# Kernel tuning notes

Hardware: AMD Instinct MI355X
Metric: run time of the kernel (lower is better)

Reference implementation:

```python
import jax, jax.numpy as jnp
import numpy as np
from jax import lax

B, N, G, K = 32, 8192, 512, 32
CH = [64, 128, 256]
EPS = 1e-5


def setup_inputs() -> dict:
    key = jax.random.key(0)
    ks = jax.random.split(key, 8)
    inp = {"points": jax.random.normal(ks[0], (B, N, 3), dtype=jnp.float32)}
    last = 3
    for li, c in enumerate(CH):
        inp[f"w{li}"] = jax.random.normal(ks[li + 1], (c, last), jnp.float32) * (1.0 / np.sqrt(last))
        inp[f"b{li}"] = jnp.zeros((c,), jnp.float32)
        inp[f"gamma{li}"] = jnp.ones((c,), jnp.float32)
        inp[f"beta{li}"] = jnp.zeros((c,), jnp.float32)
        inp[f"mean{li}"] = jnp.zeros((c,), jnp.float32)
        inp[f"var{li}"] = jnp.ones((c,), jnp.float32)
        last = c
    return inp


def _fps(xyz, npoint):
    # farthest point sampling: xyz [B,N,3] -> indices [B, npoint]
    b, n, _ = xyz.shape
    first = jnp.zeros((b,), jnp.int32)

    def step(carry, _):
        mindist, last_idx = carry
        last = jnp.take_along_axis(xyz, last_idx[:, None, None], axis=1)  # [B,1,3]
        d = jnp.sum((xyz - last) ** 2, axis=-1)  # [B,N]
        mindist = jnp.minimum(mindist, d)
        nxt = jnp.argmax(mindist, axis=-1).astype(jnp.int32)
        return (mindist, nxt), nxt

    init = (jnp.full((b, n), 1e10, jnp.float32), first)
    _, rest = lax.scan(step, init, None, length=npoint - 1)  # [npoint-1, B]
    return jnp.concatenate([first[None, :], rest], axis=0).T  # [B, npoint]


def _sample_and_group(points):
    idx_c = _fps(points, G)                                           # [B,G]
    centers = jnp.take_along_axis(points, idx_c[..., None], axis=1)   # [B,G,3]
    # kNN: squared distance [B,G,N]
    d = jnp.sum((centers[:, :, None, :] - points[:, None, :, :]) ** 2, axis=-1)
    _, idx = lax.top_k(-d, K)                                         # [B,G,K]
    grouped = jax.vmap(lambda p, i: p[i])(points, idx)                # [B,G,K,3]
    neighborhoods = grouped - centers[:, :, None, :]                  # recenter
    return neighborhoods, centers


def _mlp_maxpool(neigh, layers):
    h = neigh  # [B,G,K,C]
    for (w, b, g, be, m, v) in layers:
        h = jnp.einsum('bgkc,oc->bgko', h, w) + b       # 1x1 conv == linear
        h = (h - m) * (g / jnp.sqrt(v + EPS)) + be      # BatchNorm (inference)
        h = jax.nn.relu(h)
    return jnp.max(h, axis=(1, 2))                      # max over K then G == max over both


def reference(points, w0, b0, gamma0, beta0, mean0, var0,
              w1, b1, gamma1, beta1, mean1, var1,
              w2, b2, gamma2, beta2, mean2, var2):
    neigh, _ = _sample_and_group(points)
    layers = [(w0, b0, gamma0, beta0, mean0, var0),
              (w1, b1, gamma1, beta1, mean1, var1),
              (w2, b2, gamma2, beta2, mean2, var2)]
    return _mlp_maxpool(neigh, layers)  # [B, 256]
```

## Files before the change

### kernel.cpp

```cpp
#include <hip/hip_runtime.h>

#define B_ 32
#define N_ 8192
#define G_ 512
#define K_ 32
#define EPSF 1e-5f

typedef __attribute__((ext_vector_type(8))) short bf16x8;
typedef __attribute__((ext_vector_type(4))) float f32x4;
typedef __attribute__((ext_vector_type(2))) float f32x2;
typedef __attribute__((ext_vector_type(2))) unsigned long long u64x2;

static __device__ __forceinline__ short f2bf(float f) {
    unsigned u = __float_as_uint(f);
    u += 0x7fffu + ((u >> 16) & 1u);
    return (short)(u >> 16);
}

static __device__ __forceinline__ unsigned long long u64max(unsigned long long a,
                                                            unsigned long long b) {
    return a > b ? a : b;
}
static __device__ __forceinline__ unsigned long long u64min(unsigned long long a,
                                                            unsigned long long b) {
    return a < b ? a : b;
}

template <int CTL>
static __device__ __forceinline__ unsigned long long dpp_shr_u64(unsigned long long k) {
    const int lo = __builtin_amdgcn_mov_dpp((int)(unsigned)k, CTL, 0xf, 0xf, true);
    const int hi = __builtin_amdgcn_mov_dpp((int)(unsigned)(k >> 32), CTL, 0xf, 0xf, true);
    return ((unsigned long long)(unsigned)hi << 32) | (unsigned)lo;
}

template <int CTL>
static __device__ __forceinline__ unsigned long long dpp_upd_u64(unsigned long long k) {
    const int lo = __builtin_amdgcn_update_dpp((int)(unsigned)k, (int)(unsigned)k,
                                               CTL, 0xf, 0xf, false);
    const int hi = __builtin_amdgcn_update_dpp((int)(unsigned)(k >> 32),
                                               (int)(unsigned)(k >> 32),
                                               CTL, 0xf, 0xf, false);
    return ((unsigned long long)(unsigned)hi << 32) | (unsigned)lo;
}

__global__ __launch_bounds__(256) void prep_kernel(
    const float* __restrict__ w0, const float* __restrict__ b0,
    const float* __restrict__ g0, const float* __restrict__ be0,
    const float* __restrict__ m0, const float* __restrict__ v0,
    const float* __restrict__ w1, const float* __restrict__ b1,
    const float* __restrict__ g1, const float* __restrict__ be1,
    const float* __restrict__ m1, const float* __restrict__ v1,
    const float* __restrict__ w2, const float* __restrict__ b2,
    const float* __restrict__ g2, const float* __restrict__ be2,
    const float* __restrict__ m2, const float* __restrict__ v2,
    float* __restrict__ W0b, float* __restrict__ b1b, float* __restrict__ b2b,
    short* __restrict__ W1b, short* __restrict__ W2b) {
    const int t = threadIdx.x;
    if (t < 64) {
        const float sc = g0[t] / sqrtf(v0[t] + EPSF);
        W0b[t * 4 + 0] = w0[t * 3 + 0] * sc;
        W0b[t * 4 + 1] = w0[t * 3 + 1] * sc;
        W0b[t * 4 + 2] = w0[t * 3 + 2] * sc;
        W0b[t * 4 + 3] = (b0[t] - m0[t]) * sc + be0[t];
    }
    if (t < 128) b1b[t] = (b1[t] - m1[t]) * (g1[t] / sqrtf(v1[t] + EPSF)) + be1[t];
    if (t < 256) b2b[t] = (b2[t] - m2[t]) * (g2[t] / sqrtf(v2[t] + EPSF)) + be2[t];
    for (int i = t; i < 128 * 64; i += 256) {
        const int o = i >> 6;
        const float sc = g1[o] / sqrtf(v1[o] + EPSF);
        W1b[i] = f2bf(w1[i] * sc);
    }
    for (int i = t; i < 256 * 128; i += 256) {
        const int o = i >> 7;
        const float sc = g2[o] / sqrtf(v2[o] + EPSF);
        W2b[i] = f2bf(w2[i] * sc);
    }
}

__global__ __launch_bounds__(256) void fps_kernel(const float* __restrict__ pts,
                                                  float* __restrict__ centers) {
    __shared__ float4 sxyz[N_];
    __shared__ __align__(16) unsigned long long rowkeys[2][16];

    const int b = blockIdx.x;
    const int t = threadIdx.x;
    const int l = t & 63;
    const int w = t >> 6;
    const float* p = pts + (size_t)b * (N_ * 3);

    f32x2 px[16], py[16], pz[16], md[16];
#pragma unroll
    for (int i = 0; i < 16; ++i) {
        const int i0 = t + (2 * i) * 256;
        const int i1 = i0 + 256;
        px[i] = f32x2{p[3 * i0 + 0], p[3 * i1 + 0]};
        py[i] = f32x2{p[3 * i0 + 1], p[3 * i1 + 1]};
        pz[i] = f32x2{p[3 * i0 + 2], p[3 * i1 + 2]};
        sxyz[i0] = make_float4(px[i][0], py[i][0], pz[i][0], 0.0f);
        sxyz[i1] = make_float4(px[i][1], py[i][1], pz[i][1], 0.0f);
        md[i] = f32x2{1e10f, 1e10f};
    }
    __syncthreads();

    if (t == 0) {
        float* c = centers + (size_t)b * (G_ * 3);
        c[0] = px[0][0]; c[1] = py[0][0]; c[2] = pz[0][0];
    }
    const float4 c0 = sxyz[0];
    float lx = c0.x, ly = c0.y, lz = c0.z;
    const int pay0 = 8191 - t;

    for (int g = 1; g < G_; ++g) {
        const f32x2 nlx = {-lx, -lx};
        const f32x2 nly = {-ly, -ly};
        const f32x2 nlz = {-lz, -lz};
        float m_best = -1.0f;
        int j_best = 0;
        {
#pragma clang fp contract(off)
#pragma unroll
            for (int i = 0; i < 16; ++i) {
                const f32x2 dx = px[i] + nlx;
                const f32x2 dy = py[i] + nly;
                const f32x2 dz = pz[i] + nlz;
                const f32x2 d = (dx * dx + dy * dy) + dz * dz;
                const f32x2 m = __builtin_elementwise_min(md[i], d);
                md[i] = m;
                const bool c0_ = m[0] > m_best;
                m_best = c0_ ? m[0] : m_best;
                j_best = c0_ ? 2 * i : j_best;
                const bool c1_ = m[1] > m_best;
                m_best = c1_ ? m[1] : m_best;
                j_best = c1_ ? 2 * i + 1 : j_best;
            }
        }
        unsigned long long key =
            ((unsigned long long)__float_as_uint(m_best) << 13) |
            (unsigned long long)(unsigned)(pay0 - (j_best << 8));

        key = u64max(key, dpp_shr_u64<0x111>(key));
        key = u64max(key, dpp_shr_u64<0x112>(key));
        key = u64max(key, dpp_shr_u64<0x114>(key));
        key = u64max(key, dpp_shr_u64<0x118>(key));
        if ((l & 15) == 15) rowkeys[g & 1][w * 4 + (l >> 4)] = key;
        __syncthreads();

        const u64x2* rk = (const u64x2*)&rowkeys[g & 1][0];
        const u64x2 k2 = rk[l & 7];
        unsigned long long kk = u64max(k2[0], k2[1]);
        kk = u64max(kk, dpp_shr_u64<0x111>(kk));
        kk = u64max(kk, dpp_shr_u64<0x112>(kk));
        kk = u64max(kk, dpp_shr_u64<0x114>(kk));
        const unsigned blo =
            (unsigned)__builtin_amdgcn_readlane((int)(unsigned)kk, 7);
        const int last = 8191 - (int)(blo & 0x1FFFu);

        const float4 cc = sxyz[last];
        lx = cc.x; ly = cc.y; lz = cc.z;
        if (t == 0) {
            float* c = centers + ((size_t)b * G_ + g) * 3;
            c[0] = lx; c[1] = ly; c[2] = lz;
        }
    }
}

__global__ __launch_bounds__(256) void knn_kernel(const float* __restrict__ pts,
                                                  const float* __restrict__ centers,
                                                  float* __restrict__ neigh) {
    __shared__ unsigned long long wkeys[4][32];
    __shared__ int midx[32];

    const int cid = blockIdx.x;
    const int b = cid >> 9;
    const int t = threadIdx.x;
    const int w = t >> 6;
    const int l = t & 63;
    const float* p = pts + (size_t)b * (N_ * 3);
    const float* c = centers + (size_t)cid * 3;
    const float cx = c[0], cy = c[1], cz = c[2];

    const int iy0 = (w << 11) + l;

    unsigned int db[32];
#pragma unroll
    for (int i = 0; i < 32; ++i) {
        const int idx = iy0 + (i << 6);
        const float dx = __fsub_rn(p[3 * idx + 0], cx);
        const float dy = __fsub_rn(p[3 * idx + 1], cy);
        const float dz = __fsub_rn(p[3 * idx + 2], cz);
        const float d = __fadd_rn(__fadd_rn(__fmul_rn(dx, dx), __fmul_rn(dy, dy)),
                                  __fmul_rn(dz, dz));
        db[i] = __float_as_uint(d);
    }

    unsigned int excl = 0u;
    unsigned long long gm0, gm1, gm2, gm3;

#define KNN_SCAN_GROUP(G, DEST)                                               \
    {                                                                         \
        unsigned long long nm = ~0ull;                                        \
        _Pragma("unroll") for (int j = 0; j < 8; ++j) {                       \
            const int i = ((G) << 3) + j;                                     \
            if (!(excl & (1u << i))) {                                        \
                const unsigned long long k2 =                                 \
                    ((unsigned long long)db[i] << 13) |                       \
                    (unsigned long long)(unsigned)(iy0 + (i << 6));           \
                nm = (nm < k2) ? nm : k2;                                     \
            }                                                                 \
        }                                                                     \
        DEST = nm;                                                            \
    }

    KNN_SCAN_GROUP(0, gm0)
    KNN_SCAN_GROUP(1, gm1)
    KNN_SCAN_GROUP(2, gm2)
    KNN_SCAN_GROUP(3, gm3)
    unsigned long long lkey = u64min(u64min(gm0, gm1), u64min(gm2, gm3));

    for (int r = 0; r < K_; ++r) {
        unsigned long long x = lkey;
        x = u64min(x, dpp_upd_u64<0x111>(x));
        x = u64min(x, dpp_upd_u64<0x112>(x));
        x = u64min(x, dpp_upd_u64<0x114>(x));
        x = u64min(x, dpp_upd_u64<0x118>(x));
        x = u64min(x, dpp_upd_u64<0x142>(x));
        x = u64min(x, dpp_upd_u64<0x143>(x));
        const unsigned blo = (unsigned)__builtin_amdgcn_readlane((int)(unsigned)x, 63);
        const unsigned bhi =
            (unsigned)__builtin_amdgcn_readlane((int)(unsigned)(x >> 32), 63);
        const unsigned long long best = ((unsigned long long)bhi << 32) | blo;

        if (best == lkey) {
            const int i = ((int)(best & 0x1FFFull) >> 6) & 31;
            excl |= 1u << i;
            switch (i >> 3) {
                case 0: KNN_SCAN_GROUP(0, gm0) break;
                case 1: KNN_SCAN_GROUP(1, gm1) break;
                case 2: KNN_SCAN_GROUP(2, gm2) break;
                default: KNN_SCAN_GROUP(3, gm3) break;
            }
            lkey = u64min(u64min(gm0, gm1), u64min(gm2, gm3));
        }
        if (l == 0) wkeys[w][r] = best;
    }
#undef KNN_SCAN_GROUP
    __syncthreads();

    if (t < 128) {
        const int wv = t >> 5;
        const int pos = t & 31;
        const unsigned long long mykey = wkeys[wv][pos];
        int rank = pos;
#pragma unroll
        for (int d = 1; d < 4; ++d) {
            const int ol = (wv + d) & 3;
            int cnt = 0;
#pragma unroll
            for (int s = 32; s >= 1; s >>= 1) {
                const int n = cnt + s;
                if (n <= 32 && wkeys[ol][n - 1] < mykey) cnt = n;
            }
            rank += cnt;
        }
        if (rank < 32) midx[rank] = (int)(mykey & 0x1FFFull);
    }
    __syncthreads();

    if (t < 32) {
        const int idx = midx[t];
        float* o3 = neigh + (((size_t)cid * K_) + t) * 3;
        o3[0] = __fsub_rn(p[3 * idx + 0], cx);
        o3[1] = __fsub_rn(p[3 * idx + 1], cy);
        o3[2] = __fsub_rn(p[3 * idx + 2], cz);
    }
}

__global__ __launch_bounds__(512) void mlp_kernel(
    const float* __restrict__ neigh, const float* __restrict__ W0b,
    const float* __restrict__ b1b, const float* __restrict__ b2b,
    const short* __restrict__ W1b, const short* __restrict__ W2b,
    float* __restrict__ out) {
    __shared__ bf16x8 lw1v[1024];
    __shared__ bf16x8 lw2v[4096];
    __shared__ bf16x8 lh2v[8 * 512];
    __shared__ float lw0[256];
    __shared__ float lb1[128];
    __shared__ float lb2[256];
    __shared__ float colmax[256];

    const int t = threadIdx.x;
    const int w = t >> 6;
    const int l = t & 63;
    const int lr = l & 15;
    const int lg = l >> 4;

    {
        char* d1 = (char*)lw1v;
        for (int i = t; i < 1024; i += 512) {
            const int d = i * 16;
            const int src = d ^ ((((unsigned)d >> 7) & 7) << 4);
            *(bf16x8*)(d1 + d) = *(const bf16x8*)((const char*)W1b + src);
        }
        char* d2 = (char*)lw2v;
        for (int i = t; i < 4096; i += 512) {
            const int d = i * 16;
            const int src = d ^ ((((unsigned)d >> 8) & 7) << 4);
            *(bf16x8*)(d2 + d) = *(const bf16x8*)((const char*)W2b + src);
        }
        if (t < 256) lw0[t] = W0b[t];
        if (t < 128) lb1[t] = b1b[t];
        if (t < 256) lb2[t] = b2b[t];
        if (t < 256) colmax[t] = 0.0f;
    }
    __syncthreads();

    const size_t pbase = (size_t)blockIdx.x * 256 + w * 32;
    bf16x8 a1[2][2];
#pragma unroll
    for (int m = 0; m < 2; ++m) {
        const float* pp = neigh + (pbase + m * 16 + lr) * 3;
        const float x0 = pp[0], x1 = pp[1], x2 = pp[2];
#pragma unroll
        for (int s = 0; s < 2; ++s) {
            bf16x8 v;
#pragma unroll
            for (int j = 0; j < 8; ++j) {
                const int c = s * 32 + lg * 8 + j;
                const float4 wv = *(const float4*)&lw0[c * 4];
                float val = fmaf(x2, wv.z, fmaf(x1, wv.y, x0 * wv.x)) + wv.w;
                v[j] = f2bf(fmaxf(val, 0.0f));
            }
            a1[m][s] = v;
        }
    }

    const f32x4 vzero = {0.f, 0.f, 0.f, 0.f};
    f32x4 acc2[2][8];
#pragma unroll
    for (int m = 0; m < 2; ++m)
#pragma unroll
        for (int n = 0; n < 8; ++n) acc2[m][n] = vzero;

    const char* w1p = (const char*)lw1v;
#pragma unroll
    for (int s = 0; s < 2; ++s) {
#pragma unroll
        for (int n = 0; n < 8; ++n) {
            const int o = n * 16 + lr;
            int byte = o * 128 + s * 64 + lg * 16;
            byte ^= ((o & 7) << 4);
            const bf16x8 bfr = *(const bf16x8*)(w1p + byte);
            acc2[0][n] = __builtin_amdgcn_mfma_f32_16x16x32_bf16(a1[0][s], bfr, acc2[0][n], 0, 0, 0);
            acc2[1][n] = __builtin_amdgcn_mfma_f32_16x16x32_bf16(a1[1][s], bfr, acc2[1][n], 0, 0, 0);
        }
    }

    char* myh2 = (char*)(lh2v + w * 512);
#pragma unroll
    for (int m = 0; m < 2; ++m)
#pragma unroll
        for (int n = 0; n < 8; ++n) {
            const int o = n * 16 + lr;
            const float bb = lb1[o];
#pragma unroll
            for (int q = 0; q < 4; ++q) {
                const int row = m * 16 + lg * 4 + q;
                int byte = row * 256 + o * 2;
                byte ^= ((row & 7) << 4);
                *(short*)(myh2 + byte) = f2bf(fmaxf(acc2[m][n][q] + bb, 0.0f));
            }
        }

    f32x4 acc3[2][16];
#pragma unroll
    for (int m = 0; m < 2; ++m)
#pragma unroll
        for (int n = 0; n < 16; ++n) acc3[m][n] = vzero;

    const char* w2p = (const char*)lw2v;
#pragma unroll
    for (int s = 0; s < 4; ++s) {
        bf16x8 a[2];
#pragma unroll
        for (int m = 0; m < 2; ++m) {
            const int row = m * 16 + lr;
            int byte = row * 256 + s * 64 + lg * 16;
            byte ^= ((row & 7) << 4);
            a[m] = *(const bf16x8*)(myh2 + byte);
        }
#pragma unroll
        for (int n = 0; n < 16; ++n) {
            const int o = n * 16 + lr;
            int byte = o * 256 + s * 64 + lg * 16;
            byte ^= ((o & 7) << 4);
            const bf16x8 bfr = *(const bf16x8*)(w2p + byte);
            acc3[0][n] = __builtin_amdgcn_mfma_f32_16x16x32_bf16(a[0], bfr, acc3[0][n], 0, 0, 0);
            acc3[1][n] = __builtin_amdgcn_mfma_f32_16x16x32_bf16(a[1], bfr, acc3[1][n], 0, 0, 0);
        }
    }

#pragma unroll
    for (int n = 0; n < 16; ++n) {
        const int o = n * 16 + lr;
        const float bb = lb2[o];
        float mx = 0.0f;
#pragma unroll
        for (int m = 0; m < 2; ++m)
#pragma unroll
            for (int q = 0; q < 4; ++q) mx = fmaxf(mx, acc3[m][n][q] + bb);
        mx = fmaxf(mx, 0.0f);
        mx = fmaxf(mx, __shfl_xor(mx, 16, 64));
        mx = fmaxf(mx, __shfl_xor(mx, 32, 64));
        if (lg == 0) atomicMax((unsigned int*)&colmax[o], __float_as_uint(mx));
    }
    __syncthreads();
    if (t < 256) {
        const int b = (int)(blockIdx.x >> 6);
        atomicMax((unsigned int*)out + b * 256 + t, __float_as_uint(colmax[t]));
    }
}

extern "C" void kernel_launch(void* const* d_in, const int* in_sizes, int n_in,
                              void* d_out, int out_size, void* d_ws, size_t ws_size,
                              hipStream_t stream) {
    const float* pts = (const float*)d_in[0];
    const float* w0 = (const float*)d_in[1];
    const float* b0 = (const float*)d_in[2];
    const float* g0 = (const float*)d_in[3];
    const float* be0 = (const float*)d_in[4];
    const float* m0 = (const float*)d_in[5];
    const float* v0 = (const float*)d_in[6];
    const float* w1 = (const float*)d_in[7];
    const float* b1 = (const float*)d_in[8];
    const float* g1 = (const float*)d_in[9];
    const float* be1 = (const float*)d_in[10];
    const float* m1 = (const float*)d_in[11];
    const float* v1 = (const float*)d_in[12];
    const float* w2 = (const float*)d_in[13];
    const float* b2 = (const float*)d_in[14];
    const float* g2 = (const float*)d_in[15];
    const float* be2 = (const float*)d_in[16];
    const float* m2 = (const float*)d_in[17];
    const float* v2 = (const float*)d_in[18];

    char* ws = (char*)d_ws;
    float* centers = (float*)ws;
    float* neigh = (float*)(ws + (size_t)262144);
    char* wb = ws + (size_t)6553600;
    float* W0b = (float*)(wb + 0);
    float* b1b = (float*)(wb + 1024);
    float* b2b = (float*)(wb + 1536);
    short* W1b = (short*)(wb + 2560);
    short* W2b = (short*)(wb + 2560 + 16384);

    hipMemsetAsync(d_out, 0, (size_t)out_size * sizeof(float), stream);
    prep_kernel<<<1, 256, 0, stream>>>(w0, b0, g0, be0, m0, v0,
                                       w1, b1, g1, be1, m1, v1,
                                       w2, b2, g2, be2, m2, v2,
                                       W0b, b1b, b2b, W1b, W2b);
    fps_kernel<<<B_, 256, 0, stream>>>(pts, centers);
    knn_kernel<<<B_ * G_, 256, 0, stream>>>(pts, centers, neigh);
    mlp_kernel<<<(B_ * G_ * K_) / 256, 512, 0, stream>>>(
        neigh, W0b, b1b, b2b, W1b, W2b, (float*)d_out);
}
```

Baseline: 926.9 us.

## Carry winner coordinates through FPS argmax reduction instead of LDS lookup

The FPS kernel no longer keeps all points in shared memory. It carries each candidate's xyz through a tree reduction and the DPP cross-lane max alongside the key, then reads the new center straight from lane 15. This drops a dependent LDS load after the barrier on the serial per-iteration critical path, and the per-thread argmax becomes a tree rather than a sequential chain. In exchange it needs more DPP moves and selects per step, and more registers for the per-element candidate arrays.

New measurement: 2.587 ms. 2.79x slower.

```diff
diff --git a/kernel.cpp b/kernel.cpp
--- a/kernel.cpp
+++ b/kernel.cpp
@@ -24,13 +24,6 @@
 static __device__ __forceinline__ unsigned long long u64min(unsigned long long a,
                                                             unsigned long long b) {
     return a < b ? a : b;
-}
-
-template <int CTL>
-static __device__ __forceinline__ unsigned long long dpp_shr_u64(unsigned long long k) {
-    const int lo = __builtin_amdgcn_mov_dpp((int)(unsigned)k, CTL, 0xf, 0xf, true);
-    const int hi = __builtin_amdgcn_mov_dpp((int)(unsigned)(k >> 32), CTL, 0xf, 0xf, true);
-    return ((unsigned long long)(unsigned)hi << 32) | (unsigned)lo;
 }
 
 template <int CTL>
@@ -41,6 +34,23 @@
                                                (int)(unsigned)(k >> 32),
                                                CTL, 0xf, 0xf, false);
     return ((unsigned long long)(unsigned)hi << 32) | (unsigned)lo;
+}
+
+template <int CTL>
+static __device__ __forceinline__ void tuple_max_step(unsigned long long& key,
+                                                      float& x, float& y, float& z) {
+    const unsigned long long nk = dpp_upd_u64<CTL>(key);
+    const int nxi = __builtin_amdgcn_update_dpp(__float_as_int(x), __float_as_int(x),
+                                                CTL, 0xf, 0xf, false);
+    const int nyi = __builtin_amdgcn_update_dpp(__float_as_int(y), __float_as_int(y),
+                                                CTL, 0xf, 0xf, false);
+    const int nzi = __builtin_amdgcn_update_dpp(__float_as_int(z), __float_as_int(z),
+                                                CTL, 0xf, 0xf, false);
+    const bool c = nk > key;
+    key = c ? nk : key;
+    x = c ? __int_as_float(nxi) : x;
+    y = c ? __int_as_float(nyi) : y;
+    z = c ? __int_as_float(nzi) : z;
 }
 
 __global__ __launch_bounds__(256) void prep_kernel(
@@ -79,8 +89,9 @@
 
 __global__ __launch_bounds__(256) void fps_kernel(const float* __restrict__ pts,
                                                   float* __restrict__ centers) {
-    __shared__ float4 sxyz[N_];
-    __shared__ __align__(16) unsigned long long rowkeys[2][16];
+    __shared__ __align__(16) unsigned long long rowAB[2][16][2];
+    __shared__ float rowC[2][16];
+    __shared__ float4 c0s;
 
     const int b = blockIdx.x;
     const int t = threadIdx.x;
@@ -96,67 +107,81 @@
         px[i] = f32x2{p[3 * i0 + 0], p[3 * i1 + 0]};
         py[i] = f32x2{p[3 * i0 + 1], p[3 * i1 + 1]};
         pz[i] = f32x2{p[3 * i0 + 2], p[3 * i1 + 2]};
-        sxyz[i0] = make_float4(px[i][0], py[i][0], pz[i][0], 0.0f);
-        sxyz[i1] = make_float4(px[i][1], py[i][1], pz[i][1], 0.0f);
         md[i] = f32x2{1e10f, 1e10f};
     }
-    __syncthreads();
-
     if (t == 0) {
         float* c = centers + (size_t)b * (G_ * 3);
         c[0] = px[0][0]; c[1] = py[0][0]; c[2] = pz[0][0];
-    }
-    const float4 c0 = sxyz[0];
-    float lx = c0.x, ly = c0.y, lz = c0.z;
+        c0s = make_float4(px[0][0], py[0][0], pz[0][0], 0.0f);
+    }
+    __syncthreads();
+    float lx = c0s.x, ly = c0s.y, lz = c0s.z;
     const int pay0 = 8191 - t;
 
     for (int g = 1; g < G_; ++g) {
-        const f32x2 nlx = {-lx, -lx};
-        const f32x2 nly = {-ly, -ly};
-        const f32x2 nlz = {-lz, -lz};
-        float m_best = -1.0f;
-        int j_best = 0;
+        float v[16], wx[16], wy[16], wz[16];
+        int jj[16];
         {
 #pragma clang fp contract(off)
 #pragma unroll
             for (int i = 0; i < 16; ++i) {
-                const f32x2 dx = px[i] + nlx;
-                const f32x2 dy = py[i] + nly;
-                const f32x2 dz = pz[i] + nlz;
+                const f32x2 dx = px[i] + f32x2{-lx, -lx};
+                const f32x2 dy = py[i] + f32x2{-ly, -ly};
+                const f32x2 dz = pz[i] + f32x2{-lz, -lz};
                 const f32x2 d = (dx * dx + dy * dy) + dz * dz;
                 const f32x2 m = __builtin_elementwise_min(md[i], d);
                 md[i] = m;
-                const bool c0_ = m[0] > m_best;
-                m_best = c0_ ? m[0] : m_best;
-                j_best = c0_ ? 2 * i : j_best;
-                const bool c1_ = m[1] > m_best;
-                m_best = c1_ ? m[1] : m_best;
-                j_best = c1_ ? 2 * i + 1 : j_best;
+                const bool c = m[1] > m[0];
+                v[i] = c ? m[1] : m[0];
+                jj[i] = (i << 1) | (c ? 1 : 0);
+                wx[i] = c ? px[i][1] : px[i][0];
+                wy[i] = c ? py[i][1] : py[i][0];
+                wz[i] = c ? pz[i][1] : pz[i][0];
+            }
+        }
+#pragma unroll
+        for (int s = 1; s < 16; s <<= 1) {
+#pragma unroll
+            for (int k = 0; k < 16; k += 2 * s) {
+                const bool c = v[k + s] > v[k];
+                v[k] = c ? v[k + s] : v[k];
+                jj[k] = c ? jj[k + s] : jj[k];
+                wx[k] = c ? wx[k + s] : wx[k];
+                wy[k] = c ? wy[k + s] : wy[k];
+                wz[k] = c ? wz[k + s] : wz[k];
             }
         }
         unsigned long long key =
-            ((unsigned long long)__float_as_uint(m_best) << 13) |
-            (unsigned long long)(unsigned)(pay0 - (j_best << 8));
-
-        key = u64max(key, dpp_shr_u64<0x111>(key));
-        key = u64max(key, dpp_shr_u64<0x112>(key));
-        key = u64max(key, dpp_shr_u64<0x114>(key));
-        key = u64max(key, dpp_shr_u64<0x118>(key));
-        if ((l & 15) == 15) rowkeys[g & 1][w * 4 + (l >> 4)] = key;
+            ((unsigned long long)__float_as_uint(v[0]) << 13) |
+            (unsigned long long)(unsigned)(pay0 - (jj[0] << 8));
+        float x = wx[0], y = wy[0], z = wz[0];
+
+        tuple_max_step<0x111>(key, x, y, z);
+        tuple_max_step<0x112>(key, x, y, z);
+        tuple_max_step<0x114>(key, x, y, z);
+        tuple_max_step<0x118>(key, x, y, z);
+        if ((l & 15) == 15) {
+            const int row = w * 4 + (l >> 4);
+            u64x2 kv;
+            kv[0] = key;
+            kv[1] = ((unsigned long long)__float_as_uint(y) << 32) | __float_as_uint(x);
+            *(u64x2*)&rowAB[g & 1][row][0] = kv;
+            rowC[g & 1][row] = z;
+        }
         __syncthreads();
 
-        const u64x2* rk = (const u64x2*)&rowkeys[g & 1][0];
-        const u64x2 k2 = rk[l & 7];
-        unsigned long long kk = u64max(k2[0], k2[1]);
-        kk = u64max(kk, dpp_shr_u64<0x111>(kk));
-        kk = u64max(kk, dpp_shr_u64<0x112>(kk));
-        kk = u64max(kk, dpp_shr_u64<0x114>(kk));
-        const unsigned blo =
-            (unsigned)__builtin_amdgcn_readlane((int)(unsigned)kk, 7);
-        const int last = 8191 - (int)(blo & 0x1FFFu);
-
-        const float4 cc = sxyz[last];
-        lx = cc.x; ly = cc.y; lz = cc.z;
+        const u64x2 kv = *(const u64x2*)&rowAB[g & 1][l & 15][0];
+        unsigned long long k2 = kv[0];
+        float x2 = __uint_as_float((unsigned)kv[1]);
+        float y2 = __uint_as_float((unsigned)(kv[1] >> 32));
+        float z2 = rowC[g & 1][l & 15];
+        tuple_max_step<0x111>(k2, x2, y2, z2);
+        tuple_max_step<0x112>(k2, x2, y2, z2);
+        tuple_max_step<0x114>(k2, x2, y2, z2);
+        tuple_max_step<0x118>(k2, x2, y2, z2);
+        lx = __int_as_float(__builtin_amdgcn_readlane(__float_as_int(x2), 15));
+        ly = __int_as_float(__builtin_amdgcn_readlane(__float_as_int(y2), 15));
+        lz = __int_as_float(__builtin_amdgcn_readlane(__float_as_int(z2), 15));
         if (t == 0) {
             float* c = centers + ((size_t)b * G_ + g) * 3;
             c[0] = lx; c[1] = ly; c[2] = lz;
```
